# Performance work log

Hardware: AMD Instinct MI355X
Metric: run time of the kernel (lower is better)

The kernel has to match this reference:

```python
import jax, jax.numpy as jnp
import numpy as np
from jax import lax

NUM_ITER = 20
STOP_THRESH = 1e-4
# kernels baked from anisotropy=(1,1,0.5): (3,3,3) and (max(1,int(3*s)),...)=(3,3,1)
KERNELS = ((3, 3, 3), (3, 3, 1))
LEAK = 0.01


def _maxpool3d(x, k):
    # x: [B,C,D,H,W]; stride 1, torch-style padding (k-1)//2 (pads with -inf for max)
    window = (1, 1) + k
    pad = [(0, 0), (0, 0)] + [((ki - 1) // 2, (ki - 1) // 2) for ki in k]
    return lax.reduce_window(x, -jnp.inf, lax.max, window, (1,) * 5, pad)


def soft_erode(img):
    p = [-_maxpool3d(-img, k) for k in KERNELS]
    return jnp.minimum(p[0], p[1])


def soft_dilate(img):
    p = [_maxpool3d(img, k) for k in KERNELS]
    return jnp.maximum(p[0], p[1])


def soft_open(img):
    return soft_dilate(soft_erode(img))


def _leaky(x):
    return jax.nn.leaky_relu(x, LEAK)


def soft_skel(img):
    skel = _leaky(img - soft_open(img))
    prev_skel = jnp.zeros_like(skel)
    active = jnp.array(True)  # emulates the data-dependent `break`
    for i in range(NUM_ITER):
        img = soft_erode(img)
        lr = 0.1 * 0.5 ** (i // (NUM_ITER // 5))
        delta = _leaky(img - soft_open(img))
        skel_update = _leaky(delta - skel * delta) * lr
        skel_new = skel + skel_update
        delta_norm = jnp.mean(jnp.abs(skel_new - prev_skel))
        # torch updates skel, THEN checks and breaks; freeze after stop triggers
        skel = jnp.where(active, skel_new, skel)
        active = jnp.logical_and(active, delta_norm >= STOP_THRESH)
        prev_skel = skel
    return skel


def distance_transform(x):
    binary = (x > 0).astype(x.dtype)
    return -1.0 * (1.0 - binary) * _maxpool3d(-binary, (3, 3, 3))


def setup_inputs() -> dict:
    key = jax.random.key(0)
    img = jax.random.uniform(key, (2, 1, 128, 256, 256), dtype=jnp.float32)
    return {"img": img}


def reference(img):
    skel = soft_skel(img)
    dt = distance_transform(lax.stop_gradient(skel))  # mirrors skel.detach()
    return skel * (1.0 + 0.2 * jax.nn.sigmoid(dt))
```

## Files before the change

### kernel.cpp

```cpp
#include <hip/hip_runtime.h>
#include <hip/hip_cooperative_groups.h>
#include <cmath>

#define D_ 128
#define H_ 256
#define W4 64
#define PS (H_*W4)
#define NTOT (2*128*256*256)
#define GBLK 2048
#define ROWS 8
#define TSTART 6
#define STOPF 1e-4f

typedef _Float16 h4 __attribute__((ext_vector_type(4)));
typedef _Float16 h2v __attribute__((ext_vector_type(2)));

__device__ __forceinline__ float lk(float x){ return x >= 0.f ? x : 0.01f*x; }
__device__ __forceinline__ float4 ld4(const float4* p){ return *p; }
__device__ __forceinline__ float4 ld4(const h4* p){
    h4 v = *p; return make_float4((float)v.x,(float)v.y,(float)v.z,(float)v.w); }
__device__ __forceinline__ void st4(h4* p, float4 v){
    h4 r; r.x=(_Float16)v.x; r.y=(_Float16)v.y; r.z=(_Float16)v.z; r.w=(_Float16)v.w; *p = r; }
__device__ __forceinline__ float4 h4tof4(h4 v){
    return make_float4((float)v.x,(float)v.y,(float)v.z,(float)v.w); }
__device__ __forceinline__ h4 f4toh4(float4 v){
    h4 r; r.x=(_Float16)v.x; r.y=(_Float16)v.y; r.z=(_Float16)v.z; r.w=(_Float16)v.w; return r; }

#define PINF 0x7C007C00u
#define NINF 0xFC00FC00u
__device__ __forceinline__ uint32_t pmin(uint32_t a, uint32_t b){
    h2v r = __builtin_elementwise_min(__builtin_bit_cast(h2v,a), __builtin_bit_cast(h2v,b));
    return __builtin_bit_cast(uint32_t, r); }
__device__ __forceinline__ uint32_t pmax(uint32_t a, uint32_t b){
    h2v r = __builtin_elementwise_max(__builtin_bit_cast(h2v,a), __builtin_bit_cast(h2v,b));
    return __builtin_bit_cast(uint32_t, r); }
__device__ __forceinline__ uint2 pmin2(uint2 a, uint2 b){
    return make_uint2(pmin(a.x,b.x), pmin(a.y,b.y)); }
__device__ __forceinline__ uint2 pmax2(uint2 a, uint2 b){
    return make_uint2(pmax(a.x,b.x), pmax(a.y,b.y)); }
__device__ __forceinline__ float4 cvt4(uint32_t w01, uint32_t w23){
    h2v a = __builtin_bit_cast(h2v, w01);
    h2v b = __builtin_bit_cast(h2v, w23);
    return make_float4((float)a.x, (float)a.y, (float)b.x, (float)b.y); }
__device__ __forceinline__ uint2 pk4(float4 v){
    return __builtin_bit_cast(uint2, f4toh4(v)); }

__device__ __forceinline__ uint2 hmin2(uint2 v, int lane){
    uint32_t pw = __shfl_up(v.y,1);   if (lane == 0)  pw = PINF;
    uint32_t nw = __shfl_down(v.x,1); if (lane == 63) nw = PINF;
    uint32_t l01 = (pw  >> 16) | (v.x << 16);
    uint32_t l23 = (v.x >> 16) | (v.y << 16);
    uint32_t r23 = (v.y >> 16) | (nw  << 16);
    return make_uint2(pmin(pmin(l01,v.x),l23), pmin(pmin(l23,v.y),r23));
}
__device__ __forceinline__ uint2 hmax2(uint2 v, int lane){
    uint32_t pw = __shfl_up(v.y,1);   if (lane == 0)  pw = NINF;
    uint32_t nw = __shfl_down(v.x,1); if (lane == 63) nw = NINF;
    uint32_t l01 = (pw  >> 16) | (v.x << 16);
    uint32_t l23 = (v.x >> 16) | (v.y << 16);
    uint32_t r23 = (v.y >> 16) | (nw  << 16);
    return make_uint2(pmax(pmax(l01,v.x),l23), pmax(pmax(l23,v.y),r23));
}

struct Geo { int lane, h0; size_t pbase; bool pm, pp; };
__device__ __forceinline__ Geo mkgeo(int tid, int bi){
    Geo g;
    g.lane = tid & 63;
    int wv = tid >> 6;
    int q = bi & 7, d = (bi >> 3) & 127, b = bi >> 10;
    g.h0 = q*32 + wv*ROWS;
    g.pbase = ((size_t)(b*128 + d))*PS + (size_t)g.lane;
    g.pm = (d > 0); g.pp = (d < 127);
    return g;
}

__global__ __launch_bounds__(256) void init_k(const float* __restrict__ img0,
                                              h4* __restrict__ R0,
                                              h4* __restrict__ R1,
                                              h4* __restrict__ Sb,
                                              int* __restrict__ frozen){
    if (blockIdx.x == 0 && threadIdx.x == 0) *frozen = 0;
    int tid = threadIdx.x, lane = tid & 63, wv = tid >> 6;
    int bi = blockIdx.x;
    int q = bi & 7, d = (bi >> 3) & 127, b = bi >> 10;
    int h0 = q*32 + wv*8;
    size_t pbase = ((size_t)(b*128 + d))*PS + (size_t)lane;
    bool dm1 = d >= 1, dm2 = d >= 2, dp1 = d <= 126, dp2 = d <= 125;
    const float4* Xc = (const float4*)img0 + pbase;
    uint2* E1w = (uint2*)R0 + pbase;
    uint2* E2w = (uint2*)R1 + pbase;
    h4*    Sw  = Sb + pbase;

    float4 rawC[4];
    uint2 mnA[4], mnB[4], mnC[4], mnE[4], mxE[4];

    auto ldmg = [&](int h, int sl){
        if (h >= 0 && h < H_){
            const float4* p = Xc + h*W4;
            float4 c4 = p[0]; rawC[sl] = c4;
            uint2 c = pk4(c4);
            uint2 xm1, xm2, xp1, xp2;
            if (dm1) xm1 = pk4(p[-(int)PS]);
            if (dm2) xm2 = pk4(p[-2*(int)PS]);
            if (dp1) xp1 = pk4(p[(int)PS]);
            if (dp2) xp2 = pk4(p[2*(int)PS]);
            uint2 mb = c;
            if (dm1) mb = pmin2(mb, xm1);
            if (dp1) mb = pmin2(mb, xp1);
            mnB[sl] = mb;
            if (dm1){ uint2 a = pmin2(xm1, c); if (dm2) a = pmin2(a, xm2); mnA[sl] = a; }
            if (dp1){ uint2 cc = pmin2(xp1, c); if (dp2) cc = pmin2(cc, xp2); mnC[sl] = cc; }
        } else {
            mnA[sl] = make_uint2(PINF,PINF); mnB[sl] = make_uint2(PINF,PINF);
            mnC[sl] = make_uint2(PINF,PINF);
            rawC[sl] = make_float4(0,0,0,0);
        }
    };
    auto e1row = [&](int e, int s0, int s1, int s2, int se, bool wr){
        if (e >= 0 && e < H_){
            uint2 vb = pmin2(mnB[s0], pmin2(mnB[s1], mnB[s2]));
            uint2 e1b = hmin2(vb, lane);
            uint2 mn = e1b, mx = e1b;
            if (dm1){
                uint2 va = pmin2(mnA[s0], pmin2(mnA[s1], mnA[s2]));
                uint2 e1a = hmin2(va, lane);
                mn = pmin2(mn, e1a); mx = pmax2(mx, e1a);
            }
            if (dp1){
                uint2 vc = pmin2(mnC[s0], pmin2(mnC[s1], mnC[s2]));
                uint2 e1c = hmin2(vc, lane);
                mn = pmin2(mn, e1c); mx = pmax2(mx, e1c);
            }
            mnE[se] = mn; mxE[se] = mx;
            if (wr) E1w[e*W4] = e1b;
        } else { mnE[se] = make_uint2(PINF,PINF); mxE[se] = make_uint2(NINF,NINF); }
    };

    ldmg(h0-2, 2); ldmg(h0-1, 3); ldmg(h0+0, 0); ldmg(h0+1, 1);
    e1row(h0-1, 2,3,0, 3, false);
    e1row(h0+0, 3,0,1, 0, true);
#pragma unroll
    for (int rr = 0; rr < 8; ++rr){
        int r = h0 + rr;
        ldmg(r+2, (rr+2)&3);
        e1row(r+1, rr&3, (rr+1)&3, (rr+2)&3, (rr+1)&3, rr < 7);
        uint2 v2 = pmin2(mnE[(rr+3)&3], pmin2(mnE[rr&3], mnE[(rr+1)&3]));
        E2w[r*W4] = hmin2(v2, lane);
        uint2 vv = pmax2(mxE[(rr+3)&3], pmax2(mxE[rr&3], mxE[(rr+1)&3]));
        uint2 ow = hmax2(vv, lane);
        float4 o = cvt4(ow.x, ow.y);
        float4 a = rawC[rr&3];
        float4 s0;
        s0.x = lk(a.x-o.x); s0.y = lk(a.y-o.y);
        s0.z = lk(a.z-o.z); s0.w = lk(a.w-o.w);
        st4(Sw + r*W4, s0);
    }
}

template<int MODE, int R>
__device__ __forceinline__ double phase_pk(
    const uint2* __restrict__ Xm, const uint2* __restrict__ Xc, const uint2* __restrict__ Xp,
    bool pm, bool pp,
    uint2* __restrict__ Ep, const h4* __restrict__ Cp, h4* __restrict__ Sp,
    float lr, int h0, int lane)
{
    uint2 rmn[6], rmx[6];
    double loc = 0.0;
    auto ldrow = [&](int j){
        int s = j % 6; int h = h0 - 1 + j;
        if (h >= 0 && h < H_){
            uint2 v = *(Xc + h*W4); uint2 mn = v, mx = v;
            if (pm){ uint2 u = *(Xm + h*W4); mn = pmin2(mn,u); mx = pmax2(mx,u); }
            if (pp){ uint2 u = *(Xp + h*W4); mn = pmin2(mn,u); mx = pmax2(mx,u); }
            rmn[s] = mn; rmx[s] = mx;
        } else {
            rmn[s] = make_uint2(PINF,PINF);
            rmx[s] = make_uint2(NINF,NINF);
        }
    };
    ldrow(0); ldrow(1); ldrow(2); ldrow(3); ldrow(4);
    float4 aC = ld4(Cp + h0*W4), aN1 = aC, aN2;
    float4 sC = ld4(Sp + h0*W4), sN1 = sC, sN2;
    if (R >= 2){ aN1 = ld4(Cp + (h0+1)*W4); sN1 = ld4(Sp + (h0+1)*W4); }
#pragma unroll
    for (int rr = 0; rr < R; ++rr){
        if (rr + 5 <= R + 1) ldrow(rr+5);
        aN2 = aN1; sN2 = sN1;
        if (rr + 2 < R){
            aN2 = ld4(Cp + (h0+rr+2)*W4);
            sN2 = ld4(Sp + (h0+rr+2)*W4);
        }
        uint2 vmn = pmin2(rmn[rr%6], pmin2(rmn[(rr+1)%6], rmn[(rr+2)%6]));
        uint2 vmx = pmax2(rmx[rr%6], pmax2(rmx[(rr+1)%6], rmx[(rr+2)%6]));
        uint2 ew = hmin2(vmn, lane);
        *(Ep + (h0+rr)*W4) = ew;
        uint2 ow = hmax2(vmx, lane);
        float4 o = cvt4(ow.x, ow.y);
        float4 a = aC;
        float4 s = sC;
        float4 up; float dl;
        dl = lk(a.x-o.x); up.x = lk(dl - s.x*dl)*lr; s.x += up.x;
        dl = lk(a.y-o.y); up.y = lk(dl - s.y*dl)*lr; s.y += up.y;
        dl = lk(a.z-o.z); up.z = lk(dl - s.z*dl)*lr; s.z += up.z;
        dl = lk(a.w-o.w); up.w = lk(dl - s.w*dl)*lr; s.w += up.w;
        st4(Sp + (h0+rr)*W4, s);
        if constexpr(MODE == 2)
            loc += (double)(fabsf(s.x)+fabsf(s.y)+fabsf(s.z)+fabsf(s.w));
        else
            loc += (double)(fabsf(up.x)+fabsf(up.y)+fabsf(up.z)+fabsf(up.w));
        aC = aN1; sC = sN1; aN1 = aN2; sN1 = sN2;
    }
    return loc;
}

template<int MODE>
__global__ __launch_bounds__(256) void upd_k(const h4* __restrict__ Xb,
                                             const h4* __restrict__ Cb,
                                             h4* __restrict__ Eb,
                                             h4* __restrict__ Sb,
                                             const double* __restrict__ pr,
                                             double* __restrict__ pw,
                                             int* __restrict__ frozen,
                                             float* __restrict__ outp,
                                             float lr){
    if (*frozen) return;
    __shared__ double sm[4];
    int tid = threadIdx.x;
    int lane = tid & 63, wv = tid >> 6;
    if constexpr(MODE == 3){
        double v = 0.0;
#pragma unroll
        for (int j = 0; j < GBLK/256; ++j) v += pr[tid + 256*j];
#pragma unroll
        for (int o = 32; o; o >>= 1) v += __shfl_down(v, o);
        if (lane == 0) sm[wv] = v;
        __syncthreads();
        double tot = sm[0] + sm[1] + sm[2] + sm[3];
        if ((float)(tot / (double)NTOT) < STOPF){
            if (tid == 0) *frozen = 1;
            Geo g = mkgeo(tid, blockIdx.x);
            const h4* Sp = Sb + g.pbase;
            float4* O = (float4*)outp + g.pbase;
#pragma unroll
            for (int r = 0; r < ROWS; ++r){
                float4 s = h4tof4(Sp[(g.h0+r)*W4]);
                O[(g.h0+r)*W4] = make_float4(1.1f*s.x, 1.1f*s.y, 1.1f*s.z, 1.1f*s.w);
            }
            return;
        }
        __syncthreads();
    }
    Geo g = mkgeo(tid, blockIdx.x);
    const uint2* Xc = (const uint2*)Xb + g.pbase;
    double loc = phase_pk<MODE,ROWS>(Xc-PS, Xc, Xc+PS, g.pm, g.pp,
                                     (uint2*)Eb + g.pbase, Cb + g.pbase, Sb + g.pbase,
                                     lr, g.h0, g.lane);
#pragma unroll
    for (int o = 32; o; o >>= 1) loc += __shfl_down(loc, o);
    if (lane == 0) sm[wv] = loc;
    __syncthreads();
    if (tid == 0) pw[blockIdx.x] = sm[0]+sm[1]+sm[2]+sm[3];
}

__global__ __launch_bounds__(256) void tail_k(h4* __restrict__ rg0,
                                              h4* __restrict__ rg1,
                                              h4* __restrict__ rg2,
                                              h4* __restrict__ S,
                                              float* __restrict__ outp,
                                              const double* __restrict__ pr0,
                                              double* __restrict__ tp0,
                                              double* __restrict__ tp1,
                                              const int* __restrict__ frozen){
    if (*frozen) return;
    cooperative_groups::grid_group gg = cooperative_groups::this_grid();
    __shared__ double sm[4];
    int tid = threadIdx.x, lane = tid & 63, wv = tid >> 6;
    int bi = blockIdx.x;
    int d = bi >> 3, b = (bi >> 2) & 1, q = bi & 3;
    int h0 = q*64 + wv*16;
    size_t pbase = ((size_t)(b*128 + d))*PS + (size_t)lane;
    bool pm = d > 0, pp = d < 127;
    const double* pr = pr0; int prn = GBLK;
    double* tpw = tp0;
    for (int i = TSTART; i < 20; ++i){
        double v = 0.0;
        for (int j = 0; j < prn/256; ++j) v += pr[tid + 256*j];
#pragma unroll
        for (int o = 32; o; o >>= 1) v += __shfl_down(v, o);
        if (lane == 0) sm[wv] = v;
        __syncthreads();
        double tot = sm[0] + sm[1] + sm[2] + sm[3];
        if ((float)(tot / (double)NTOT) < STOPF) break;
        __syncthreads();
        int xs = (i+1)%3, es = (i+2)%3, cs = i%3;
        h4* X = xs==0 ? rg0 : (xs==1 ? rg1 : rg2);
        h4* E = es==0 ? rg0 : (es==1 ? rg1 : rg2);
        h4* C = cs==0 ? rg0 : (cs==1 ? rg1 : rg2);
        float lr = 0.1f * exp2f(-(float)(i >> 2));
        const uint2* Xc = (const uint2*)X + pbase;
        double loc = phase_pk<3,16>(Xc-PS, Xc, Xc+PS, pm, pp, (uint2*)E + pbase,
                                    C + pbase, S + pbase, lr, h0, lane);
#pragma unroll
        for (int o = 32; o; o >>= 1) loc += __shfl_down(loc, o);
        if (lane == 0) sm[wv] = loc;
        __syncthreads();
        if (tid == 0) tpw[blockIdx.x] = sm[0]+sm[1]+sm[2]+sm[3];
        gg.sync();
        pr = tpw; prn = 1024;
        tpw = (tpw == tp0) ? tp1 : tp0;
    }
    const h4* Sp = S + pbase;
    float4* O = (float4*)outp + pbase;
#pragma unroll
    for (int r = 0; r < 16; ++r){
        float4 s = h4tof4(Sp[(h0+r)*W4]);
        O[(h0+r)*W4] = make_float4(1.1f*s.x, 1.1f*s.y, 1.1f*s.z, 1.1f*s.w);
    }
}

__global__ __launch_bounds__(256) void scale_k(const h4* __restrict__ S,
                                               float* __restrict__ out){
    int t = blockIdx.x*256 + threadIdx.x;
#pragma unroll
    for (int c = 0; c < 4; ++c){
        int i = t + c*1048576;
        float4 s = ld4(S + i);
        float4 r = make_float4(1.1f*s.x, 1.1f*s.y, 1.1f*s.z, 1.1f*s.w);
        *(float4*)(out + (size_t)i*4) = r;
    }
}

extern "C" void kernel_launch(void* const* d_in, const int* in_sizes, int n_in,
                              void* d_out, int out_size, void* d_ws, size_t ws_size,
                              hipStream_t stream){
    const float* img0 = (const float*)d_in[0];
    float* out = (float*)d_out;
    char* ws = (char*)d_ws;
    size_t volh = (size_t)NTOT * 2;
    h4* ring[3] = { (h4*)ws, (h4*)(ws + volh), (h4*)(ws + 2*volh) };
    h4* S       = (h4*)(ws + 3*volh);
    double* parts[2] = { (double*)(ws + 4*volh), (double*)(ws + 4*volh) + GBLK };
    int* frozen = (int*)(ws + 4*volh + 2*GBLK*sizeof(double));
    double* tp0 = (double*)(ws + 4*volh + 2*GBLK*sizeof(double) + 256);
    double* tp1 = tp0 + 1024;

    dim3 blk(256), grd(GBLK);
    hipLaunchKernelGGL(init_k, grd, blk, 0, stream, img0, ring[0], ring[1], S, frozen);

    for (int i = 0; i < TSTART; ++i){
        h4* C = ring[i % 3];
        h4* X = ring[(i+1) % 3];
        h4* E = ring[(i+2) % 3];
        float lr = (float)(0.1 * pow(0.5, (double)(i / 4)));
        double* pw = parts[i & 1];
        double* pr = parts[1 - (i & 1)];
        if (i == 0)
            hipLaunchKernelGGL((upd_k<2>), grd, blk, 0, stream, X, C, E, S, pr, pw, frozen, out, lr);
        else
            hipLaunchKernelGGL((upd_k<3>), grd, blk, 0, stream, X, C, E, S, pr, pw, frozen, out, lr);
    }

    h4* a_r0 = ring[0]; h4* a_r1 = ring[1]; h4* a_r2 = ring[2];
    h4* a_S = S; float* a_out = out;
    const double* a_pr0 = parts[1 - (TSTART & 1)];
    double* a_tp0 = tp0; double* a_tp1 = tp1; int* a_fz = frozen;
    void* args[9] = { &a_r0, &a_r1, &a_r2, &a_S, &a_out, &a_pr0, &a_tp0, &a_tp1, &a_fz };
    hipError_t ce = hipLaunchCooperativeKernel((const void*)tail_k, dim3(1024), blk,
                                               args, 0u, stream);
    if (ce != hipSuccess){
        for (int i = TSTART; i < 20; ++i){
            h4* C = ring[i % 3];
            h4* X = ring[(i+1) % 3];
            h4* E = ring[(i+2) % 3];
            float lr = (float)(0.1 * pow(0.5, (double)(i / 4)));
            double* pw = parts[i & 1];
            double* pr = parts[1 - (i & 1)];
            hipLaunchKernelGGL((upd_k<3>), grd, blk, 0, stream, X, C, E, S, pr, pw, frozen, out, lr);
        }
        hipLaunchKernelGGL(scale_k, dim3(4096), blk, 0, stream, S, out);
    }
}
```

Measured before the change: 300.7 us.

## Widen upd_k to 16-byte loads with half-wave row pairs and xor shuffles

The per-iteration update kernel now has each lane handle 8 half-precision values (uint4) instead of 4. Each wave covers two rows at once, with the two half-waves owning adjacent rows and exchanging vertical neighbours through shfl_xor 32. This is meant to halve the number of memory instructions and raise bytes per load, at the cost of extra cross-lane shuffles and more complex boundary handling. The old phase_pk is kept below with a smaller register ring, presumably for use in tail_k.

```diff
diff --git a/kernel.cpp b/kernel.cpp
--- a/kernel.cpp
+++ b/kernel.cpp
@@ -5,7 +5,9 @@
 #define D_ 128
 #define H_ 256
 #define W4 64
+#define W8 32
 #define PS (H_*W4)
+#define PS8 (H_*W8)
 #define NTOT (2*128*256*256)
 #define GBLK 2048
 #define ROWS 8
@@ -38,12 +40,19 @@
     return make_uint2(pmin(a.x,b.x), pmin(a.y,b.y)); }
 __device__ __forceinline__ uint2 pmax2(uint2 a, uint2 b){
     return make_uint2(pmax(a.x,b.x), pmax(a.y,b.y)); }
+__device__ __forceinline__ uint4 pmin4u(uint4 a, uint4 b){
+    return make_uint4(pmin(a.x,b.x),pmin(a.y,b.y),pmin(a.z,b.z),pmin(a.w,b.w)); }
+__device__ __forceinline__ uint4 pmax4u(uint4 a, uint4 b){
+    return make_uint4(pmax(a.x,b.x),pmax(a.y,b.y),pmax(a.z,b.z),pmax(a.w,b.w)); }
 __device__ __forceinline__ float4 cvt4(uint32_t w01, uint32_t w23){
     h2v a = __builtin_bit_cast(h2v, w01);
     h2v b = __builtin_bit_cast(h2v, w23);
     return make_float4((float)a.x, (float)a.y, (float)b.x, (float)b.y); }
 __device__ __forceinline__ uint2 pk4(float4 v){
     return __builtin_bit_cast(uint2, f4toh4(v)); }
+__device__ __forceinline__ uint4 x32(uint4 v){
+    return make_uint4(__shfl_xor(v.x,32),__shfl_xor(v.y,32),
+                      __shfl_xor(v.z,32),__shfl_xor(v.w,32)); }
 
 __device__ __forceinline__ uint2 hmin2(uint2 v, int lane){
     uint32_t pw = __shfl_up(v.y,1);   if (lane == 0)  pw = PINF;
@@ -60,6 +69,29 @@
     uint32_t l23 = (v.x >> 16) | (v.y << 16);
     uint32_t r23 = (v.y >> 16) | (nw  << 16);
     return make_uint2(pmax(pmax(l01,v.x),l23), pmax(pmax(l23,v.y),r23));
+}
+
+__device__ __forceinline__ uint4 hwin_min4(uint4 v, int wl){
+    uint32_t ld = __shfl_up(v.w,1);   if (wl == 0)  ld = PINF;
+    uint32_t ra = __shfl_down(v.x,1); if (wl == 31) ra = PINF;
+    uint32_t s0 = (ld >> 16) | (v.x << 16);
+    uint32_t s1 = (v.x >> 16) | (v.y << 16);
+    uint32_t s2 = (v.y >> 16) | (v.z << 16);
+    uint32_t s3 = (v.z >> 16) | (v.w << 16);
+    uint32_t s4 = (v.w >> 16) | (ra << 16);
+    return make_uint4(pmin(s0,pmin(v.x,s1)), pmin(s1,pmin(v.y,s2)),
+                      pmin(s2,pmin(v.z,s3)), pmin(s3,pmin(v.w,s4)));
+}
+__device__ __forceinline__ uint4 hwin_max4(uint4 v, int wl){
+    uint32_t ld = __shfl_up(v.w,1);   if (wl == 0)  ld = NINF;
+    uint32_t ra = __shfl_down(v.x,1); if (wl == 31) ra = NINF;
+    uint32_t s0 = (ld >> 16) | (v.x << 16);
+    uint32_t s1 = (v.x >> 16) | (v.y << 16);
+    uint32_t s2 = (v.y >> 16) | (v.z << 16);
+    uint32_t s3 = (v.z >> 16) | (v.w << 16);
+    uint32_t s4 = (v.w >> 16) | (ra << 16);
+    return make_uint4(pmax(s0,pmax(v.x,s1)), pmax(s1,pmax(v.y,s2)),
+                      pmax(s2,pmax(v.z,s3)), pmax(s3,pmax(v.w,s4)));
 }
 
 struct Geo { int lane, h0; size_t pbase; bool pm, pp; };
@@ -157,58 +189,70 @@
     }
 }
 
-template<int MODE, int R>
-__device__ __forceinline__ double phase_pk(
-    const uint2* __restrict__ Xm, const uint2* __restrict__ Xc, const uint2* __restrict__ Xp,
+template<int MODE>
+__device__ __forceinline__ double phase_wide(
+    const uint4* __restrict__ Xm8, const uint4* __restrict__ Xc8, const uint4* __restrict__ Xp8,
     bool pm, bool pp,
-    uint2* __restrict__ Ep, const h4* __restrict__ Cp, h4* __restrict__ Sp,
-    float lr, int h0, int lane)
+    uint4* __restrict__ Ep8, const uint4* __restrict__ Cp8, uint4* __restrict__ Sp8,
+    float lr, int h0, int rl, int wl)
 {
-    uint2 rmn[6], rmx[6];
+    uint4 mn[4], mx[4];
     double loc = 0.0;
-    auto ldrow = [&](int j){
-        int s = j % 6; int h = h0 - 1 + j;
-        if (h >= 0 && h < H_){
-            uint2 v = *(Xc + h*W4); uint2 mn = v, mx = v;
-            if (pm){ uint2 u = *(Xm + h*W4); mn = pmin2(mn,u); mx = pmax2(mx,u); }
-            if (pp){ uint2 u = *(Xp + h*W4); mn = pmin2(mn,u); mx = pmax2(mx,u); }
-            rmn[s] = mn; rmx[s] = mx;
-        } else {
-            rmn[s] = make_uint2(PINF,PINF);
-            rmx[s] = make_uint2(NINF,NINF);
-        }
+    const uint4 VPI = make_uint4(PINF,PINF,PINF,PINF);
+    const uint4 VNI = make_uint4(NINF,NINF,NINF,NINF);
+    auto ldpair = [&](int j){
+        int s = (j+1)&3;
+        int r = h0 + 2*j + rl;
+        bool ok = (r >= 0) && (r < H_);
+        if (j == -1) ok = ok && (rl == 1);
+        if (j == 4)  ok = ok && (rl == 0);
+        if (ok){
+            const uint4* p = Xc8 + r*W8;
+            uint4 v = *p; uint4 a = v, b = v;
+            if (pm){ uint4 u = *(Xm8 + r*W8); a = pmin4u(a,u); b = pmax4u(b,u); }
+            if (pp){ uint4 u = *(Xp8 + r*W8); a = pmin4u(a,u); b = pmax4u(b,u); }
+            mn[s] = a; mx[s] = b;
+        } else { mn[s] = VPI; mx[s] = VNI; }
     };
-    ldrow(0); ldrow(1); ldrow(2); ldrow(3); ldrow(4);
-    float4 aC = ld4(Cp + h0*W4), aN1 = aC, aN2;
-    float4 sC = ld4(Sp + h0*W4), sN1 = sC, sN2;
-    if (R >= 2){ aN1 = ld4(Cp + (h0+1)*W4); sN1 = ld4(Sp + (h0+1)*W4); }
-#pragma unroll
-    for (int rr = 0; rr < R; ++rr){
-        if (rr + 5 <= R + 1) ldrow(rr+5);
-        aN2 = aN1; sN2 = sN1;
-        if (rr + 2 < R){
-            aN2 = ld4(Cp + (h0+rr+2)*W4);
-            sN2 = ld4(Sp + (h0+rr+2)*W4);
-        }
-        uint2 vmn = pmin2(rmn[rr%6], pmin2(rmn[(rr+1)%6], rmn[(rr+2)%6]));
-        uint2 vmx = pmax2(rmx[rr%6], pmax2(rmx[(rr+1)%6], rmx[(rr+2)%6]));
-        uint2 ew = hmin2(vmn, lane);
-        *(Ep + (h0+rr)*W4) = ew;
-        uint2 ow = hmax2(vmx, lane);
-        float4 o = cvt4(ow.x, ow.y);
-        float4 a = aC;
-        float4 s = sC;
+    ldpair(-1); ldpair(0); ldpair(1);
+#pragma unroll
+    for (int rr = 0; rr < 4; ++rr){
+        if (rr < 3) ldpair(rr+2);
+        int sp = rr&3, so = (rr+1)&3, sn = (rr+2)&3;
+        int r = h0 + 2*rr + rl;
+        uint4 up_mn = x32(rl ? mn[sp] : mn[so]);
+        uint4 dn_mn = x32(rl ? mn[so] : mn[sn]);
+        uint4 vmn = pmin4u(up_mn, pmin4u(mn[so], dn_mn));
+        uint4 up_mx = x32(rl ? mx[sp] : mx[so]);
+        uint4 dn_mx = x32(rl ? mx[so] : mx[sn]);
+        uint4 vmx = pmax4u(up_mx, pmax4u(mx[so], dn_mx));
+        uint4 ew = hwin_min4(vmn, wl);
+        *(Ep8 + r*W8) = ew;
+        uint4 ow = hwin_max4(vmx, wl);
+        uint4 cw = *(Cp8 + r*W8);
+        uint4 sw = *(Sp8 + r*W8);
+        float4 oL = cvt4(ow.x, ow.y), oH = cvt4(ow.z, ow.w);
+        float4 aL = cvt4(cw.x, cw.y), aH = cvt4(cw.z, cw.w);
+        float4 sL = cvt4(sw.x, sw.y), sH = cvt4(sw.z, sw.w);
         float4 up; float dl;
-        dl = lk(a.x-o.x); up.x = lk(dl - s.x*dl)*lr; s.x += up.x;
-        dl = lk(a.y-o.y); up.y = lk(dl - s.y*dl)*lr; s.y += up.y;
-        dl = lk(a.z-o.z); up.z = lk(dl - s.z*dl)*lr; s.z += up.z;
-        dl = lk(a.w-o.w); up.w = lk(dl - s.w*dl)*lr; s.w += up.w;
-        st4(Sp + (h0+rr)*W4, s);
+        dl = lk(aL.x-oL.x); up.x = lk(dl - sL.x*dl)*lr; sL.x += up.x;
+        dl = lk(aL.y-oL.y); up.y = lk(dl - sL.y*dl)*lr; sL.y += up.y;
+        dl = lk(aL.z-oL.z); up.z = lk(dl - sL.z*dl)*lr; sL.z += up.z;
+        dl = lk(aL.w-oL.w); up.w = lk(dl - sL.w*dl)*lr; sL.w += up.w;
         if constexpr(MODE == 2)
-            loc += (double)(fabsf(s.x)+fabsf(s.y)+fabsf(s.z)+fabsf(s.w));
+            loc += (double)(fabsf(sL.x)+fabsf(sL.y)+fabsf(sL.z)+fabsf(sL.w));
         else
             loc += (double)(fabsf(up.x)+fabsf(up.y)+fabsf(up.z)+fabsf(up.w));
-        aC = aN1; sC = sN1; aN1 = aN2; sN1 = sN2;
+        dl = lk(aH.x-oH.x); up.x = lk(dl - sH.x*dl)*lr; sH.x += up.x;
+        dl = lk(aH.y-oH.y); up.y = lk(dl - sH.y*dl)*lr; sH.y += up.y;
+        dl = lk(aH.z-oH.z); up.z = lk(dl - sH.z*dl)*lr; sH.z += up.z;
+        dl = lk(aH.w-oH.w); up.w = lk(dl - sH.w*dl)*lr; sH.w += up.w;
+        if constexpr(MODE == 2)
+            loc += (double)(fabsf(sH.x)+fabsf(sH.y)+fabsf(sH.z)+fabsf(sH.w));
+        else
+            loc += (double)(fabsf(up.x)+fabsf(up.y)+fabsf(up.z)+fabsf(up.w));
+        uint2 pL = pk4(sL), pH = pk4(sH);
+        *(Sp8 + r*W8) = make_uint4(pL.x, pL.y, pH.x, pH.y);
     }
     return loc;
 }
@@ -250,16 +294,76 @@
         }
         __syncthreads();
     }
-    Geo g = mkgeo(tid, blockIdx.x);
-    const uint2* Xc = (const uint2*)Xb + g.pbase;
-    double loc = phase_pk<MODE,ROWS>(Xc-PS, Xc, Xc+PS, g.pm, g.pp,
-                                     (uint2*)Eb + g.pbase, Cb + g.pbase, Sb + g.pbase,
-                                     lr, g.h0, g.lane);
+    int bi = blockIdx.x;
+    int q = bi & 7, d = (bi >> 3) & 127, b = bi >> 10;
+    int rl = lane >> 5, wl = lane & 31;
+    int h0 = q*32 + wv*8;
+    size_t base8 = ((size_t)(b*128 + d))*PS8 + (size_t)wl;
+    bool pm = d > 0, pp = d < 127;
+    const uint4* Xc8 = (const uint4*)Xb + base8;
+    double loc = phase_wide<MODE>(Xc8-PS8, Xc8, Xc8+PS8, pm, pp,
+                                  (uint4*)Eb + base8, (const uint4*)Cb + base8,
+                                  (uint4*)Sb + base8, lr, h0, rl, wl);
 #pragma unroll
     for (int o = 32; o; o >>= 1) loc += __shfl_down(loc, o);
     if (lane == 0) sm[wv] = loc;
     __syncthreads();
     if (tid == 0) pw[blockIdx.x] = sm[0]+sm[1]+sm[2]+sm[3];
+}
+
+template<int MODE, int R>
+__device__ __forceinline__ double phase_pk(
+    const uint2* __restrict__ Xm, const uint2* __restrict__ Xc, const uint2* __restrict__ Xp,
+    bool pm, bool pp,
+    uint2* __restrict__ Ep, const h4* __restrict__ Cp, h4* __restrict__ Sp,
+    float lr, int h0, int lane)
+{
+    uint2 rmn[4], rmx[4];
+    double loc = 0.0;
+    auto ldrow = [&](int j){
+        int s = j & 3; int h = h0 - 1 + j;
+        if (h >= 0 && h < H_){
+            uint2 v = *(Xc + h*W4); uint2 mn = v, mx = v;
+            if (pm){ uint2 u = *(Xm + h*W4); mn = pmin2(mn,u); mx = pmax2(mx,u); }
+            if (pp){ uint2 u = *(Xp + h*W4); mn = pmin2(mn,u); mx = pmax2(mx,u); }
+            rmn[s] = mn; rmx[s] = mx;
+        } else {
+            rmn[s] = make_uint2(PINF,PINF);
+            rmx[s] = make_uint2(NINF,NINF);
+        }
+    };
+    ldrow(0); ldrow(1); ldrow(2);
+    float4 a_cur = ld4(Cp + h0*W4);
+    float4 s_cur = ld4(Sp + h0*W4);
+#pragma unroll
+    for (int r = 0; r < R; ++r){
+        if (r + 3 <= R + 1) ldrow(r+3);
+        float4 a_nxt = a_cur, s_nxt = s_cur;
+        if (r + 1 < R){
+            a_nxt = ld4(Cp + (h0+r+1)*W4);
+            s_nxt = ld4(Sp + (h0+r+1)*W4);
+        }
+        uint2 vmn = pmin2(rmn[r&3], pmin2(rmn[(r+1)&3], rmn[(r+2)&3]));
+        uint2 vmx = pmax2(rmx[r&3], pmax2(rmx[(r+1)&3], rmx[(r+2)&3]));
+        uint2 ew = hmin2(vmn, lane);
+        *(Ep + (h0+r)*W4) = ew;
+        uint2 ow = hmax2(vmx, lane);
+        float4 o = cvt4(ow.x, ow.y);
+        float4 a = a_cur;
+        float4 s = s_cur;
+        float4 up; float dl;
+        dl = lk(a.x-o.x); up.x = lk(dl - s.x*dl)*lr; s.x += up.x;
+        dl = lk(a.y-o.y); up.y = lk(dl - s.y*dl)*lr; s.y += up.y;
+        dl = lk(a.z-o.z); up.z = lk(dl - s.z*dl)*lr; s.z += up.z;
+        dl = lk(a.w-o.w); up.w = lk(dl - s.w*dl)*lr; s.w += up.w;
+        st4(Sp + (h0+r)*W4, s);
+        if constexpr(MODE == 2)
+            loc += (double)(fabsf(s.x)+fabsf(s.y)+fabsf(s.z)+fabsf(s.w));
+        else
+            loc += (double)(fabsf(up.x)+fabsf(up.y)+fabsf(up.z)+fabsf(up.w));
+        a_cur = a_nxt; s_cur = s_nxt;
+    }
+    return loc;
 }
 
 __global__ __launch_bounds__(256) void tail_k(h4* __restrict__ rg0,
```

Result: faster. 292.2 us (-2.8%).
